# Performance work log

Hardware: AMD Instinct MI355X
Metric: run time of the kernel (lower is better)

The kernel has to match this reference:

```python
import math
import jax, jax.numpy as jnp
import numpy as np

B, T, D_MODEL, N_HEADS = 2, 2048, 1024, 16
HEAD_DIM = D_MODEL // N_HEADS  # 64


def setup_inputs() -> dict:
    key = jax.random.key(0)
    k1, k2, k3, k4, k5 = jax.random.split(key, 5)
    x = jax.random.normal(k1, (B, T, D_MODEL), dtype=jnp.float32)
    init = 0.02
    Wq = jax.random.normal(k2, (D_MODEL, D_MODEL), dtype=jnp.float32) * init
    Wk = jax.random.normal(k3, (D_MODEL, D_MODEL), dtype=jnp.float32) * init
    Wv = jax.random.normal(k4, (D_MODEL, D_MODEL), dtype=jnp.float32) * init
    Wo = jax.random.normal(k5, (D_MODEL, D_MODEL), dtype=jnp.float32) * init
    # causal mask, broadcastable over (B, H): 1 = keep, 0 = masked
    mask = jnp.tril(jnp.ones((T, T), dtype=jnp.int32))[None, None, :, :]
    return {"x": x, "Wq": Wq, "Wk": Wk, "Wv": Wv, "Wo": Wo, "mask": mask}


def ternary_weight(W):
    # BitNet-b1.58 style ternary quantization with straight-through estimator
    scale = jnp.mean(jnp.abs(W))
    Wt = jnp.round(jnp.clip(W / (scale + 1e-8), -1.0, 1.0)) * scale
    return W + jax.lax.stop_gradient(Wt - W)


def rope_cos_sin(seq_len, dim):
    inv_freq = 1.0 / (10000.0 ** (jnp.arange(0, dim, 2, dtype=jnp.float32) / dim))
    freqs = jnp.outer(jnp.arange(seq_len, dtype=jnp.float32), inv_freq)  # [T, dim/2]
    emb = jnp.concatenate([freqs, freqs], axis=-1)  # [T, dim]
    return jnp.cos(emb)[None, None, :, :], jnp.sin(emb)[None, None, :, :]


def rotate_half(x):
    h = x.shape[-1] // 2
    return jnp.concatenate([-x[..., h:], x[..., :h]], axis=-1)


def reference(x, Wq, Wk, Wv, Wo, mask):
    Bb, Tt, C = x.shape
    H, D = N_HEADS, HEAD_DIM
    # ternary-quantized projections (bias-free)
    q = (x @ ternary_weight(Wq).T).reshape(Bb, Tt, H, D).transpose(0, 2, 1, 3)
    k = (x @ ternary_weight(Wk).T).reshape(Bb, Tt, H, D).transpose(0, 2, 1, 3)
    v = (x @ ternary_weight(Wv).T).reshape(Bb, Tt, H, D).transpose(0, 2, 1, 3)
    cos, sin = rope_cos_sin(Tt, D)  # [1,1,T,D]
    q = q * cos + rotate_half(q) * sin
    k = k * cos + rotate_half(k) * sin
    att = jnp.einsum("bhqd,bhkd->bhqk", q, k) / math.sqrt(D)
    att = jnp.where(mask == 0, -jnp.inf, att)
    att = jax.nn.softmax(att, axis=-1)  # dropout omitted (eval mode, p effectively 0)
    y = jnp.einsum("bhqk,bhkd->bhqd", att, v)
    y = y.transpose(0, 2, 1, 3).reshape(Bb, Tt, C)
    return y @ ternary_weight(Wo).T
```

## Files before the change

### kernel.cpp

```cpp
#include <hip/hip_runtime.h>
#include <math.h>

using bf16x8  = __attribute__((ext_vector_type(8))) __bf16;
using floatx4 = __attribute__((ext_vector_type(4))) float;
using ushortx8 = __attribute__((ext_vector_type(8))) unsigned short;
using ushortx4 = __attribute__((ext_vector_type(4))) unsigned short;
typedef unsigned short u16;

__device__ __forceinline__ float bf2f(u16 u) {
  unsigned int x = ((unsigned int)u) << 16;
  return __builtin_bit_cast(float, x);
}
__device__ __forceinline__ u16 f2bf(float f) {
  unsigned int x = __builtin_bit_cast(unsigned int, f);
  x += 0x7FFFu + ((x >> 16) & 1u);
  return (u16)(x >> 16);
}
__device__ __forceinline__ float fexp2(float x) { return __builtin_amdgcn_exp2f(x); }
__device__ __forceinline__ unsigned cvtpk(float lo, float hi) {
  unsigned r;
  asm("v_cvt_pk_bf16_f32 %0, %1, %2" : "=v"(r) : "v"(lo), "v"(hi));
  return r;
}
__device__ __forceinline__ float scale_of(const float* __restrict__ partials, int w) {
  float s = 0.f;
  for (int i = 0; i < 64; ++i) s += partials[w * 64 + i];
  return s * (1.f / 1048576.f);
}

#define GLDS16(SRC, DST)                                                        \
  __builtin_amdgcn_global_load_lds((const __attribute__((address_space(1))) void*)(SRC), \
                                   (__attribute__((address_space(3))) void*)(DST), 16, 0, 0)

__global__ __launch_bounds__(256) void prep_kernel(const float* __restrict__ x, u16* __restrict__ xb,
                                                   const float* W0, const float* W1,
                                                   const float* W2, const float* W3,
                                                   float* partials) {
  __shared__ float red[256];
  int tid = threadIdx.x;
  if (blockIdx.x < 2048) {
    int g = (blockIdx.x * 256 + tid) * 8;
    float4 a = *(const float4*)(x + g);
    float4 b = *(const float4*)(x + g + 4);
    ushortx8 o;
    o[0] = f2bf(a.x); o[1] = f2bf(a.y); o[2] = f2bf(a.z); o[3] = f2bf(a.w);
    o[4] = f2bf(b.x); o[5] = f2bf(b.y); o[6] = f2bf(b.z); o[7] = f2bf(b.w);
    *(ushortx8*)(xb + g) = o;
    return;
  }
  int idx = blockIdx.x - 2048;
  int bx = idx & 63, w = idx >> 6;
  const float* W = (w == 0) ? W0 : (w == 1) ? W1 : (w == 2) ? W2 : W3;
  int base = bx * 16384 + tid;
  float s = 0.f;
#pragma unroll
  for (int i = 0; i < 64; ++i) s += fabsf(W[base + i * 256]);
  red[tid] = s;
  __syncthreads();
  for (int off = 128; off > 0; off >>= 1) {
    if (tid < off) red[tid] += red[tid + off];
    __syncthreads();
  }
  if (tid == 0) partials[w * 64 + bx] = red[0];
}

__global__ __launch_bounds__(256) void quant_kernel(const float* W0, const float* W1,
                                                    const float* W2, const float* W3,
                                                    const float* partials, u16* Wt) {
  int w = blockIdx.y;
  const float* W = (w == 0) ? W0 : (w == 1) ? W1 : (w == 2) ? W2 : W3;
  u16* O = Wt + (size_t)w * (1u << 20);
  float s = scale_of(partials, w) + 1e-8f;
  int e = (blockIdx.x * 256 + threadIdx.x) * 4;
  float4 v = *(const float4*)(W + e);
  ushortx4 o;
  o[0] = f2bf(rintf(fminf(fmaxf(v.x / s, -1.f), 1.f)));
  o[1] = f2bf(rintf(fminf(fmaxf(v.y / s, -1.f), 1.f)));
  o[2] = f2bf(rintf(fminf(fmaxf(v.z / s, -1.f), 1.f)));
  o[3] = f2bf(rintf(fminf(fmaxf(v.w / s, -1.f), 1.f)));
  *(ushortx4*)(O + e) = o;
}

__global__ __launch_bounds__(256) void gemm_qkv(const u16* __restrict__ A, const u16* __restrict__ Wt,
                                                u16* __restrict__ QKV, u16* __restrict__ vt,
                                                const float* __restrict__ partials) {
  const int K = 1024;
  __shared__ __align__(16) u16 As[128][64];
  __shared__ __align__(16) u16 Bs[64][64];
  int tid = threadIdx.x;
  int wave = tid >> 6, lane = tid & 63;
  int quad = lane >> 4, l16 = lane & 15;
  int bm = blockIdx.x * 128;
  int bnc = blockIdx.y * 64;
  int mat = bnc >> 10, bn = bnc & 1023;
  int wm = wave * 32;
  floatx4 acc[2][4] = {};
  int scol = ((lane & 7) ^ ((lane >> 3) & 7)) * 8;
  const u16* ga = A  + (size_t)(bm + wave * 32 + (lane >> 3)) * K + scol;
  const u16* gb = Wt + (size_t)(bnc + wave * 16 + (lane >> 3)) * K + scol;
  int rx = (l16 & 7);
  for (int k0 = 0; k0 < K; k0 += 64) {
    __syncthreads();
#pragma unroll
    for (int i = 0; i < 4; ++i)
      GLDS16(ga + (size_t)i * 8 * K + k0, &As[wave * 32 + i * 8][0]);
#pragma unroll
    for (int i = 0; i < 2; ++i)
      GLDS16(gb + (size_t)i * 8 * K + k0, &Bs[wave * 16 + i * 8][0]);
    __syncthreads();
#pragma unroll
    for (int kk = 0; kk < 64; kk += 32) {
      int col = (((kk >> 3) + quad) ^ rx) * 8;
      bf16x8 a[2], b[4];
#pragma unroll
      for (int i = 0; i < 2; ++i)
        a[i] = __builtin_bit_cast(bf16x8, *(const ushortx8*)&As[wm + i * 16 + l16][col]);
#pragma unroll
      for (int j = 0; j < 4; ++j)
        b[j] = __builtin_bit_cast(bf16x8, *(const ushortx8*)&Bs[j * 16 + l16][col]);
#pragma unroll
      for (int i = 0; i < 2; ++i)
#pragma unroll
        for (int j = 0; j < 4; ++j)
          acc[i][j] = __builtin_amdgcn_mfma_f32_16x16x32_bf16(a[i], b[j], acc[i][j], 0, 0, 0);
    }
  }
  float sc = scale_of(partials, mat);
  if (mat < 2) {
    u16* outp = QKV + (size_t)mat * (4u << 20);
    float qs = (mat == 0) ? 0.125f * 1.4426950408889634f : 1.0f;
    float inv0 = exp2f(-(float)l16 * (13.287712379549449f / 32.f));
    float inv1 = exp2f(-(float)(16 + l16) * (13.287712379549449f / 32.f));
#pragma unroll
    for (int i = 0; i < 2; ++i)
#pragma unroll
      for (int rg = 0; rg < 4; ++rg) {
        int row = bm + wm + i * 16 + quad * 4 + rg;
        float tf = (float)(row & 2047);
#pragma unroll
        for (int j = 0; j < 2; ++j) {
          float ang = tf * (j ? inv1 : inv0);
          float s = __sinf(ang), c = __cosf(ang);
          float v1 = acc[i][j][rg] * sc, v2 = acc[i][j + 2][rg] * sc;
          int col = bn + j * 16 + l16;
          outp[(size_t)row * 1024 + col]      = f2bf((v1 * c - v2 * s) * qs);
          outp[(size_t)row * 1024 + col + 32] = f2bf((v2 * c + v1 * s) * qs);
        }
      }
  } else {
    int h = bn >> 6;
#pragma unroll
    for (int i = 0; i < 2; ++i) {
      int row0 = bm + wm + i * 16 + quad * 4;
      int b = row0 >> 11, t0 = row0 & 2047;
#pragma unroll
      for (int j = 0; j < 4; ++j) {
        int d = j * 16 + l16;
        ushortx4 o;
#pragma unroll
        for (int rg = 0; rg < 4; ++rg) o[rg] = f2bf(acc[i][j][rg] * sc);
        *(ushortx4*)(vt + (size_t)((b * 16 + h) * 64 + d) * 2048 + t0) = o;
      }
    }
  }
}

__global__ __launch_bounds__(256) void gemm_out(const u16* __restrict__ A, const u16* __restrict__ B,
                                                float* __restrict__ C, const float* __restrict__ partials) {
  const int K = 1024, N = 1024;
  __shared__ __align__(16) u16 As[128][64];
  __shared__ __align__(16) u16 Bs[64][64];
  int tid = threadIdx.x;
  int wave = tid >> 6, lane = tid & 63;
  int quad = lane >> 4, l16 = lane & 15;
  int bm = blockIdx.x * 128, bn = blockIdx.y * 64;
  int wm = (wave >> 1) * 64, wn = (wave & 1) * 32;
  floatx4 acc[4][2] = {};
  int scol = ((lane & 7) ^ ((lane >> 3) & 7)) * 8;
  const u16* ga = A + (size_t)(bm + wave * 32 + (lane >> 3)) * K + scol;
  const u16* gb = B + (size_t)(bn + wave * 16 + (lane >> 3)) * K + scol;
  int rx = (l16 & 7);
  for (int k0 = 0; k0 < K; k0 += 64) {
    __syncthreads();
#pragma unroll
    for (int i = 0; i < 4; ++i)
      GLDS16(ga + (size_t)i * 8 * K + k0, &As[wave * 32 + i * 8][0]);
#pragma unroll
    for (int i = 0; i < 2; ++i)
      GLDS16(gb + (size_t)i * 8 * K + k0, &Bs[wave * 16 + i * 8][0]);
    __syncthreads();
#pragma unroll
    for (int kk = 0; kk < 64; kk += 32) {
      int col = (((kk >> 3) + quad) ^ rx) * 8;
      bf16x8 a[4], b[2];
#pragma unroll
      for (int i = 0; i < 4; ++i)
        a[i] = __builtin_bit_cast(bf16x8, *(const ushortx8*)&As[wm + i * 16 + l16][col]);
#pragma unroll
      for (int j = 0; j < 2; ++j)
        b[j] = __builtin_bit_cast(bf16x8, *(const ushortx8*)&Bs[wn + j * 16 + l16][col]);
#pragma unroll
      for (int i = 0; i < 4; ++i)
#pragma unroll
        for (int j = 0; j < 2; ++j)
          acc[i][j] = __builtin_amdgcn_mfma_f32_16x16x32_bf16(a[i], b[j], acc[i][j], 0, 0, 0);
    }
  }
  float sc = scale_of(partials, 3);
#pragma unroll
  for (int i = 0; i < 4; ++i)
#pragma unroll
    for (int j = 0; j < 2; ++j)
#pragma unroll
      for (int rg = 0; rg < 4; ++rg) {
        int row = bm + wm + i * 16 + quad * 4 + rg;
        int col = bn + wn + j * 16 + l16;
        C[(size_t)row * N + col] = acc[i][j][rg] * sc;
      }
}

__global__ __launch_bounds__(256, 3) void attn_kernel(const u16* __restrict__ q, const u16* __restrict__ k,
                                                      const u16* __restrict__ vt, u16* __restrict__ y) {
  __shared__ __align__(16) u16 Ks[2][64][72];
  __shared__ __align__(16) u16 Vt[2][64][72];
  __shared__ __align__(16) u16 Ps[4][16][72];
  const int T = 2048, C = 1024;
  int tid = threadIdx.x;
  int wave = tid >> 6, lane = tid & 63;
  int quad = lane >> 4, l16 = lane & 15;
  int p = blockIdx.y;
  int bh = blockIdx.x;
  int b = bh >> 4, h = bh & 15;
  int wq[2];
  wq[0] = p * 64 + wave * 16;
  wq[1] = (31 - p) * 64 + wave * 16;
  int dt[2] = {p, 31 - p};
  int nkt = 32 - p;

  bf16x8 bq[2][2];
#pragma unroll
  for (int g = 0; g < 2; ++g) {
    const u16* gq = q + (size_t)(b * T + wq[g] + l16) * C + h * 64 + quad * 8;
    bq[g][0] = __builtin_bit_cast(bf16x8, *(const ushortx8*)(gq));
    bq[g][1] = __builtin_bit_cast(bf16x8, *(const ushortx8*)(gq + 32));
  }

  ushortx8 onesu;
#pragma unroll
  for (int j = 0; j < 8; ++j) onesu[j] = 0x3F80;
  bf16x8 bones = __builtin_bit_cast(bf16x8, onesu);

  int srow = tid >> 2, sc16 = (tid & 3) << 4;
  const u16* kptr  = k  + (size_t)(b * T + srow) * C + h * 64 + sc16;
  const u16* vtptr = vt + (size_t)(bh * 64 + srow) * 2048 + sc16;

  floatx4 o[2][5] = {};

  ushortx8 kra = *(const ushortx8*)kptr;
  ushortx8 krb = *(const ushortx8*)(kptr + 8);
  ushortx8 vra = *(const ushortx8*)vtptr;
  ushortx8 vrb = *(const ushortx8*)(vtptr + 8);
  *(ushortx8*)&Ks[0][srow][sc16]     = kra;
  *(ushortx8*)&Ks[0][srow][sc16 + 8] = krb;
  *(ushortx8*)&Vt[0][srow][sc16]     = vra;
  *(ushortx8*)&Vt[0][srow][sc16 + 8] = vrb;
  __syncthreads();

  for (int kt = 0; kt < nkt; ++kt) {
    int cur = kt & 1;
    bool haveNext = (kt + 1) < nkt;
    if (haveNext) {
      kra = *(const ushortx8*)(kptr + (size_t)(kt + 1) * 64 * C);
      krb = *(const ushortx8*)(kptr + (size_t)(kt + 1) * 64 * C + 8);
      vra = *(const ushortx8*)(vtptr + (kt + 1) * 64);
      vrb = *(const ushortx8*)(vtptr + (kt + 1) * 64 + 8);
    }

    bool act[2] = {kt <= dt[0], true};

    floatx4 sacc[2][4] = {};
    __builtin_amdgcn_s_setprio(1);
#pragma unroll
    for (int nt = 0; nt < 4; ++nt) {
      bf16x8 ak0 = __builtin_bit_cast(bf16x8, *(const ushortx8*)&Ks[cur][nt * 16 + l16][quad * 8]);
      bf16x8 ak1 = __builtin_bit_cast(bf16x8, *(const ushortx8*)&Ks[cur][nt * 16 + l16][32 + quad * 8]);
#pragma unroll
      for (int g = 0; g < 2; ++g)
        if (act[g]) {
          sacc[g][nt] = __builtin_amdgcn_mfma_f32_16x16x32_bf16(ak0, bq[g][0], sacc[g][nt], 0, 0, 0);
          sacc[g][nt] = __builtin_amdgcn_mfma_f32_16x16x32_bf16(ak1, bq[g][1], sacc[g][nt], 0, 0, 0);
        }
    }
    __builtin_amdgcn_s_setprio(0);

    bf16x8 ap[2][2];
#pragma unroll
    for (int g = 0; g < 2; ++g)
      if (act[g]) {
        if (kt == dt[g]) {
          int qg = wq[g] + l16;
#pragma unroll
          for (int nt = 0; nt < 4; ++nt)
#pragma unroll
            for (int rg = 0; rg < 4; ++rg)
              if (kt * 64 + nt * 16 + quad * 4 + rg > qg) sacc[g][nt][rg] = -__builtin_inff();
        }
#pragma unroll
        for (int nt = 0; nt < 4; ++nt) {
          float p0 = fexp2(sacc[g][nt][0]);
          float p1 = fexp2(sacc[g][nt][1]);
          float p2 = fexp2(sacc[g][nt][2]);
          float p3 = fexp2(sacc[g][nt][3]);
          unsigned lo = cvtpk(p0, p1);
          unsigned hi = cvtpk(p2, p3);
          *(uint2*)&Ps[wave][l16][nt * 16 + quad * 4] = make_uint2(lo, hi);
        }
        ap[g][0] = __builtin_bit_cast(bf16x8, *(const ushortx8*)&Ps[wave][l16][quad * 8]);
        ap[g][1] = __builtin_bit_cast(bf16x8, *(const ushortx8*)&Ps[wave][l16][32 + quad * 8]);
      }

    __builtin_amdgcn_s_setprio(1);
#pragma unroll
    for (int nt = 0; nt < 4; ++nt) {
      bf16x8 bv0 = __builtin_bit_cast(bf16x8, *(const ushortx8*)&Vt[cur][nt * 16 + l16][quad * 8]);
      bf16x8 bv1 = __builtin_bit_cast(bf16x8, *(const ushortx8*)&Vt[cur][nt * 16 + l16][32 + quad * 8]);
#pragma unroll
      for (int g = 0; g < 2; ++g)
        if (act[g]) {
          o[g][nt] = __builtin_amdgcn_mfma_f32_16x16x32_bf16(ap[g][0], bv0, o[g][nt], 0, 0, 0);
          o[g][nt] = __builtin_amdgcn_mfma_f32_16x16x32_bf16(ap[g][1], bv1, o[g][nt], 0, 0, 0);
        }
    }
#pragma unroll
    for (int g = 0; g < 2; ++g)
      if (act[g]) {
        o[g][4] = __builtin_amdgcn_mfma_f32_16x16x32_bf16(ap[g][0], bones, o[g][4], 0, 0, 0);
        o[g][4] = __builtin_amdgcn_mfma_f32_16x16x32_bf16(ap[g][1], bones, o[g][4], 0, 0, 0);
      }
    __builtin_amdgcn_s_setprio(0);

    if (haveNext) {
      int nb = cur ^ 1;
      *(ushortx8*)&Ks[nb][srow][sc16]     = kra;
      *(ushortx8*)&Ks[nb][srow][sc16 + 8] = krb;
      *(ushortx8*)&Vt[nb][srow][sc16]     = vra;
      *(ushortx8*)&Vt[nb][srow][sc16 + 8] = vrb;
    }
    __syncthreads();
  }

#pragma unroll
  for (int g = 0; g < 2; ++g) {
    float inv[4];
#pragma unroll
    for (int rg = 0; rg < 4; ++rg) inv[rg] = __builtin_amdgcn_rcpf(o[g][4][rg]);
#pragma unroll
    for (int nt = 0; nt < 4; ++nt)
#pragma unroll
      for (int rg = 0; rg < 4; ++rg) {
        int qg = wq[g] + quad * 4 + rg;
        int col = h * 64 + nt * 16 + l16;
        y[(size_t)(b * T + qg) * C + col] = f2bf(o[g][nt][rg] * inv[rg]);
      }
  }
}

extern "C" void kernel_launch(void* const* d_in, const int* in_sizes, int n_in,
                              void* d_out, int out_size, void* d_ws, size_t ws_size,
                              hipStream_t stream) {
  const float* x  = (const float*)d_in[0];
  const float* Wq = (const float*)d_in[1];
  const float* Wk = (const float*)d_in[2];
  const float* Wv = (const float*)d_in[3];
  const float* Wo = (const float*)d_in[4];

  char* ws = (char*)d_ws;
  float* partials = (float*)ws;
  u16* Wt  = (u16*)(ws + 4096);
  u16* xb  = (u16*)(ws + 4096 + (size_t)(8u << 20));
  u16* qb  = xb + (4u << 20);
  u16* kb  = qb + (4u << 20);
  u16* vtb = kb + (4u << 20);
  u16* yb  = vtb + (4u << 20);
  float* out = (float*)d_out;

  prep_kernel<<<2304, 256, 0, stream>>>(x, xb, Wq, Wk, Wv, Wo, partials);
  quant_kernel<<<dim3(1024, 4), 256, 0, stream>>>(Wq, Wk, Wv, Wo, partials, Wt);

  gemm_qkv<<<dim3(32, 48), 256, 0, stream>>>(xb, Wt, qb, vtb, partials);
  attn_kernel<<<dim3(32, 16), 256, 0, stream>>>(qb, kb, vtb, yb);
  gemm_out<<<dim3(32, 16), 256, 0, stream>>>(yb, Wt + 3 * (1u << 20), out, partials);
}
```

Baseline: 191.0 us.

## Stage K/V tiles with direct global-to-LDS loads and XOR-swizzled layout

```diff
diff --git a/kernel.cpp b/kernel.cpp
--- a/kernel.cpp
+++ b/kernel.cpp
@@ -221,8 +221,8 @@
 
 __global__ __launch_bounds__(256, 3) void attn_kernel(const u16* __restrict__ q, const u16* __restrict__ k,
                                                       const u16* __restrict__ vt, u16* __restrict__ y) {
-  __shared__ __align__(16) u16 Ks[2][64][72];
-  __shared__ __align__(16) u16 Vt[2][64][72];
+  __shared__ __align__(16) u16 Ks[2][64][64];
+  __shared__ __align__(16) u16 Vt[2][64][64];
   __shared__ __align__(16) u16 Ps[4][16][72];
   const int T = 2048, C = 1024;
   int tid = threadIdx.x;
@@ -250,40 +250,39 @@
   for (int j = 0; j < 8; ++j) onesu[j] = 0x3F80;
   bf16x8 bones = __builtin_bit_cast(bf16x8, onesu);
 
-  int srow = tid >> 2, sc16 = (tid & 3) << 4;
-  const u16* kptr  = k  + (size_t)(b * T + srow) * C + h * 64 + sc16;
-  const u16* vtptr = vt + (size_t)(bh * 64 + srow) * 2048 + sc16;
+  int grow = lane >> 3;
+  int gchk = ((lane & 7) ^ grow) * 8;
+  const u16* kbase = k  + (size_t)(b * T + grow) * C + h * 64 + gchk;
+  const u16* vbase = vt + (size_t)(bh * 64 + grow) * 2048 + gchk;
+
+#define STAGE_KV(BB, KT)                                                                     \
+  do {                                                                                       \
+    _Pragma("unroll")                                                                        \
+    for (int i_ = 0; i_ < 2; ++i_) {                                                         \
+      int rb_ = (wave + 4 * i_) * 8;                                                         \
+      GLDS16(kbase + (size_t)((KT) * 64 + rb_) * C, &Ks[BB][rb_][0]);                        \
+      GLDS16(vbase + (size_t)rb_ * 2048 + (KT) * 64, &Vt[BB][rb_][0]);                       \
+    }                                                                                        \
+  } while (0)
 
   floatx4 o[2][5] = {};
 
-  ushortx8 kra = *(const ushortx8*)kptr;
-  ushortx8 krb = *(const ushortx8*)(kptr + 8);
-  ushortx8 vra = *(const ushortx8*)vtptr;
-  ushortx8 vrb = *(const ushortx8*)(vtptr + 8);
-  *(ushortx8*)&Ks[0][srow][sc16]     = kra;
-  *(ushortx8*)&Ks[0][srow][sc16 + 8] = krb;
-  *(ushortx8*)&Vt[0][srow][sc16]     = vra;
-  *(ushortx8*)&Vt[0][srow][sc16 + 8] = vrb;
+  STAGE_KV(0, 0);
   __syncthreads();
+
+  int rxk = l16 & 7;
 
   for (int kt = 0; kt < nkt; ++kt) {
     int cur = kt & 1;
-    bool haveNext = (kt + 1) < nkt;
-    if (haveNext) {
-      kra = *(const ushortx8*)(kptr + (size_t)(kt + 1) * 64 * C);
-      krb = *(const ushortx8*)(kptr + (size_t)(kt + 1) * 64 * C + 8);
-      vra = *(const ushortx8*)(vtptr + (kt + 1) * 64);
-      vrb = *(const ushortx8*)(vtptr + (kt + 1) * 64 + 8);
-    }
+    if (kt + 1 < nkt) STAGE_KV(cur ^ 1, kt + 1);
 
     bool act[2] = {kt <= dt[0], true};
 
     floatx4 sacc[2][4] = {};
-    __builtin_amdgcn_s_setprio(1);
 #pragma unroll
     for (int nt = 0; nt < 4; ++nt) {
-      bf16x8 ak0 = __builtin_bit_cast(bf16x8, *(const ushortx8*)&Ks[cur][nt * 16 + l16][quad * 8]);
-      bf16x8 ak1 = __builtin_bit_cast(bf16x8, *(const ushortx8*)&Ks[cur][nt * 16 + l16][32 + quad * 8]);
+      bf16x8 ak0 = __builtin_bit_cast(bf16x8, *(const ushortx8*)&Ks[cur][nt * 16 + l16][(quad ^ rxk) * 8]);
+      bf16x8 ak1 = __builtin_bit_cast(bf16x8, *(const ushortx8*)&Ks[cur][nt * 16 + l16][((quad | 4) ^ rxk) * 8]);
 #pragma unroll
       for (int g = 0; g < 2; ++g)
         if (act[g]) {
@@ -291,7 +290,6 @@
           sacc[g][nt] = __builtin_amdgcn_mfma_f32_16x16x32_bf16(ak1, bq[g][1], sacc[g][nt], 0, 0, 0);
         }
     }
-    __builtin_amdgcn_s_setprio(0);
 
     bf16x8 ap[2][2];
 #pragma unroll
@@ -319,11 +317,10 @@
         ap[g][1] = __builtin_bit_cast(bf16x8, *(const ushortx8*)&Ps[wave][l16][32 + quad * 8]);
       }
 
-    __builtin_amdgcn_s_setprio(1);
 #pragma unroll
     for (int nt = 0; nt < 4; ++nt) {
-      bf16x8 bv0 = __builtin_bit_cast(bf16x8, *(const ushortx8*)&Vt[cur][nt * 16 + l16][quad * 8]);
-      bf16x8 bv1 = __builtin_bit_cast(bf16x8, *(const ushortx8*)&Vt[cur][nt * 16 + l16][32 + quad * 8]);
+      bf16x8 bv0 = __builtin_bit_cast(bf16x8, *(const ushortx8*)&Vt[cur][nt * 16 + l16][(quad ^ rxk) * 8]);
+      bf16x8 bv1 = __builtin_bit_cast(bf16x8, *(const ushortx8*)&Vt[cur][nt * 16 + l16][((quad | 4) ^ rxk) * 8]);
 #pragma unroll
       for (int g = 0; g < 2; ++g)
         if (act[g]) {
@@ -337,17 +334,10 @@
         o[g][4] = __builtin_amdgcn_mfma_f32_16x16x32_bf16(ap[g][0], bones, o[g][4], 0, 0, 0);
         o[g][4] = __builtin_amdgcn_mfma_f32_16x16x32_bf16(ap[g][1], bones, o[g][4], 0, 0, 0);
       }
-    __builtin_amdgcn_s_setprio(0);
-
-    if (haveNext) {
-      int nb = cur ^ 1;
-      *(ushortx8*)&Ks[nb][srow][sc16]     = kra;
-      *(ushortx8*)&Ks[nb][srow][sc16 + 8] = krb;
-      *(ushortx8*)&Vt[nb][srow][sc16]     = vra;
-      *(ushortx8*)&Vt[nb][srow][sc16 + 8] = vrb;
-    }
-    __syncthreads();
-  }
+
+    __syncthreads();
+  }
+#undef STAGE_KV
 
 #pragma unroll
   for (int g = 0; g < 2; ++g) {
```

Result: faster. 185.4 us (median of 2 runs) (-2.9%).
